# Kernel optimization log

Hardware: AMD Instinct MI355X
Metric: run time of the kernel (lower is better)

## Reference

```python
import jax, jax.numpy as jnp
import numpy as np

K = 3  # kernel size
PAD = 1  # padding (stride=1, dilation=1)


def _unfold(x, k=K, pad=PAD):
    """im2col: x [B,C,H,W] -> [B,C,k,k,H,W] (stride=1, dilation=1)."""
    B, C, H, W = x.shape
    xp = jnp.pad(x, ((0, 0), (0, 0), (pad, pad), (pad, pad)))
    # small fixed k*k loop, stacked into window dims
    rows = []
    for i in range(k):
        cols = [xp[:, :, i:i + H, j:j + W] for j in range(k)]
        rows.append(jnp.stack(cols, axis=2))  # [B,C,k,H,W]
    return jnp.stack(rows, axis=2)  # [B,C,k,k,H,W]


def setup_inputs() -> dict:
    key = jax.random.key(0)
    k1, k2, k3, k4 = jax.random.split(key, 4)
    B, C, O, H, W = 4, 64, 64, 128, 128
    inputs = jax.random.normal(k1, (B, C, H, W), dtype=jnp.float32)
    alpha = jax.random.uniform(k2, (B, 1, H, W), dtype=jnp.float32)
    fan_in = C * K * K
    weight = jax.random.normal(k3, (O, C, K, K), dtype=jnp.float32) / np.sqrt(fan_in)
    bias = jax.random.normal(k4, (O,), dtype=jnp.float32) / np.sqrt(fan_in)
    return {
        "inputs": inputs,
        "alpha": alpha,
        "weight": weight,
        "bias": bias,
        "a": jnp.float32(-4.0),
        "b": jnp.float32(4.0),
        "c": jnp.float32(1.0),
    }


def reference(inputs, alpha, weight, bias, a, b, c):
    # spatially-varying kernel from alpha: (a*x + b)*x + c on unfolded windows
    alpha_wins = _unfold(alpha)                      # [B,1,k,k,H,W]
    kernel = (a * alpha_wins + b) * alpha_wins + c   # [B,1,k,k,H,W]
    inputs_wins = _unfold(inputs)                    # [B,C,k,k,H,W]
    inputs_mul_kernel = inputs_wins * kernel         # broadcast over C
    out = jnp.einsum('ijklmn,ojkl->iomn', inputs_mul_kernel, weight)
    out = out + bias[None, :, None, None]
    return out
```

## Files before the change

kernel.cpp:

```cpp
#include <hip/hip_runtime.h>

typedef __bf16 bf16x8 __attribute__((ext_vector_type(8)));
typedef float f32x4 __attribute__((ext_vector_type(4)));

#define BB 4
#define CC 64
#define OO 64
#define HH 128
#define WW 128

__global__ __launch_bounds__(256) void prepack_kernel(
    const float* __restrict__ w, unsigned short* __restrict__ aw)
{
    int gid = blockIdx.x * 256 + threadIdx.x;
    if (gid >= 4608) return;
    int og  = gid / 1152;
    int rem = gid - og * 1152;
    int t = rem >> 6;
    int l = rem & 63;
    int q = l >> 4;
    int m = l & 15;
    int o  = og * 16 + m;
    int ij = t >> 1;
    int ch = t & 1;
    int i = ij / 3;
    int j = ij - i * 3;
    union { unsigned short u[8]; uint4 v; } pk;
#pragma unroll
    for (int jj = 0; jj < 8; ++jj) {
        int c = ch * 32 + q * 8 + jj;
        float wf = w[((o * CC + c) * 3 + i) * 3 + j];
        __bf16 h = (__bf16)wf;
        pk.u[jj] = __builtin_bit_cast(unsigned short, h);
    }
    ((uint4*)aw)[gid] = pk.v;
}

__global__ __launch_bounds__(256) void prescale_kernel(
    const float* __restrict__ in, const float* __restrict__ alpha,
    const float* __restrict__ pa, const float* __restrict__ pb, const float* __restrict__ pc,
    unsigned short* __restrict__ xs)
{
    __shared__ float trans[64][65];
    int bid = blockIdx.x;
    int xh  = bid & 1;
    int by  = bid >> 1;
    int y   = by & 127;
    int b   = by >> 7;
    int x0  = xh * 64;
    int tid = threadIdx.x;

    float A  = *pa, Bc = *pb, Cc = *pc;

    int x  = tid & 63;
    int c4 = tid >> 6;
    float av = alpha[(b * HH + y) * WW + x0 + x];
    float f  = (A * av + Bc) * av + Cc;
#pragma unroll
    for (int k = 0; k < 16; ++k) {
        int c = c4 * 16 + k;
        float v = in[((b * CC + c) * HH + y) * WW + x0 + x];
        trans[c][x] = v * f;
    }
    __syncthreads();

    int xw = tid >> 2;
    int cg = tid & 3;
    union { unsigned short u[16]; uint4 v4[2]; } pk;
#pragma unroll
    for (int k = 0; k < 16; ++k) {
        __bf16 h = (__bf16)trans[cg * 16 + k][xw];
        pk.u[k] = __builtin_bit_cast(unsigned short, h);
    }
    uint4* dst = (uint4*)(xs + (((size_t)(b * HH + y) * WW + x0 + xw) * CC + cg * 16));
    dst[0] = pk.v4[0];
    dst[1] = pk.v4[1];
}

__global__ __launch_bounds__(256, 2) void conv_kernel(
    const unsigned short* __restrict__ xs, const unsigned short* __restrict__ aw,
    const float* __restrict__ bias, float* __restrict__ out)
{
    __shared__ unsigned short tile[3 * 130 * 72];

    int n   = blockIdx.x;
    int xcd = n & 7;
    int idx = n >> 3;
    int b   = xcd >> 1;
    int y   = (xcd & 1) * 64 + idx;
    int tid = threadIdx.x;

    for (int s = tid; s < 3120; s += 256) {
        int g  = s & 7;
        int rx = s >> 3;
        int r  = rx / 130;
        int xt = rx - r * 130;
        int yy = y + r - 1;
        int xg = xt - 1;
        uint4 val = make_uint4(0u, 0u, 0u, 0u);
        if ((unsigned)yy < (unsigned)HH && (unsigned)xg < (unsigned)WW)
            val = *(const uint4*)(xs + (((size_t)(b * HH + yy) * WW + xg) * CC + g * 8));
        *(uint4*)(tile + (r * 130 + xt) * 72 + g * 8) = val;
    }
    __syncthreads();

    int wv = tid >> 6;
    int l  = tid & 63;
    int oh = wv & 1;
    int nh = wv >> 1;
    int q  = l >> 4;
    int m  = l & 15;

    f32x4 acc[2][4];
#pragma unroll
    for (int ag = 0; ag < 2; ++ag)
#pragma unroll
        for (int nf = 0; nf < 4; ++nf)
            acc[ag][nf] = (f32x4){0.f, 0.f, 0.f, 0.f};

    const uint4* awv = (const uint4*)aw + (size_t)(oh * 2) * 18 * 64 + l;

#pragma unroll 3
    for (int ij = 0; ij < 9; ++ij) {
        const int i = ij / 3;
        const int j = ij - i * 3;
#pragma unroll
        for (int ch = 0; ch < 2; ++ch) {
            const int t = ij * 2 + ch;
            bf16x8 afrag[2], bfrag[4];
#pragma unroll
            for (int ag = 0; ag < 2; ++ag)
                afrag[ag] = __builtin_bit_cast(bf16x8, awv[(ag * 18 + t) * 64]);
#pragma unroll
            for (int nf = 0; nf < 4; ++nf) {
                int xt = nh * 64 + nf * 16 + m + j;
                bfrag[nf] = __builtin_bit_cast(bf16x8,
                    *(const uint4*)(tile + (i * 130 + xt) * 72 + ch * 32 + q * 8));
            }
#pragma unroll
            for (int ag = 0; ag < 2; ++ag)
#pragma unroll
                for (int nf = 0; nf < 4; ++nf)
                    acc[ag][nf] = __builtin_amdgcn_mfma_f32_16x16x32_bf16(
                        afrag[ag], bfrag[nf], acc[ag][nf], 0, 0, 0);
        }
    }

#pragma unroll
    for (int ag = 0; ag < 2; ++ag) {
#pragma unroll
        for (int r = 0; r < 4; ++r) {
            int o = (oh * 2 + ag) * 16 + q * 4 + r;
            float bv = bias[o];
#pragma unroll
            for (int nf = 0; nf < 4; ++nf) {
                int x = nh * 64 + nf * 16 + m;
                out[((size_t)(b * OO + o) * HH + y) * WW + x] = acc[ag][nf][r] + bv;
            }
        }
    }
}

extern "C" void kernel_launch(void* const* d_in, const int* in_sizes, int n_in,
                              void* d_out, int out_size, void* d_ws, size_t ws_size,
                              hipStream_t stream) {
    const float* inputs = (const float*)d_in[0];
    const float* alpha  = (const float*)d_in[1];
    const float* weight = (const float*)d_in[2];
    const float* bias   = (const float*)d_in[3];
    const float* pa     = (const float*)d_in[4];
    const float* pb     = (const float*)d_in[5];
    const float* pc     = (const float*)d_in[6];
    float* out = (float*)d_out;

    unsigned short* aw = (unsigned short*)d_ws;
    unsigned short* xs = (unsigned short*)((char*)d_ws + 131072);

    prepack_kernel<<<18, 256, 0, stream>>>(weight, aw);
    prescale_kernel<<<BB * HH * 2, 256, 0, stream>>>(inputs, alpha, pa, pb, pc, xs);
    conv_kernel<<<BB * HH, 256, 0, stream>>>(xs, aw, bias, out);
}
```

Before: 96.45 us.

## Fuse alpha prescale and bf16 transpose into the conv kernel tile load

Removes the separate prescale kernel and its bf16 NHWC intermediate buffer. Each conv block now reads the three fp32 input rows directly, applies the alpha polynomial, transposes through a small shared buffer, and writes bf16 into the shared tile, with the halo columns zeroed explicitly. This saves a kernel launch and the intermediate write and read, but each input row is now loaded and converted by three blocks. The staging loop also adds 24 block-wide barriers with little overlap between loads and conversion.

```diff
diff --git a/kernel.cpp b/kernel.cpp
--- a/kernel.cpp
+++ b/kernel.cpp
@@ -36,52 +36,14 @@
     ((uint4*)aw)[gid] = pk.v;
 }
 
-__global__ __launch_bounds__(256) void prescale_kernel(
+__global__ __launch_bounds__(256, 2) void fused_conv_kernel(
     const float* __restrict__ in, const float* __restrict__ alpha,
+    const unsigned short* __restrict__ aw, const float* __restrict__ bias,
     const float* __restrict__ pa, const float* __restrict__ pb, const float* __restrict__ pc,
-    unsigned short* __restrict__ xs)
-{
-    __shared__ float trans[64][65];
-    int bid = blockIdx.x;
-    int xh  = bid & 1;
-    int by  = bid >> 1;
-    int y   = by & 127;
-    int b   = by >> 7;
-    int x0  = xh * 64;
-    int tid = threadIdx.x;
-
-    float A  = *pa, Bc = *pb, Cc = *pc;
-
-    int x  = tid & 63;
-    int c4 = tid >> 6;
-    float av = alpha[(b * HH + y) * WW + x0 + x];
-    float f  = (A * av + Bc) * av + Cc;
-#pragma unroll
-    for (int k = 0; k < 16; ++k) {
-        int c = c4 * 16 + k;
-        float v = in[((b * CC + c) * HH + y) * WW + x0 + x];
-        trans[c][x] = v * f;
-    }
-    __syncthreads();
-
-    int xw = tid >> 2;
-    int cg = tid & 3;
-    union { unsigned short u[16]; uint4 v4[2]; } pk;
-#pragma unroll
-    for (int k = 0; k < 16; ++k) {
-        __bf16 h = (__bf16)trans[cg * 16 + k][xw];
-        pk.u[k] = __builtin_bit_cast(unsigned short, h);
-    }
-    uint4* dst = (uint4*)(xs + (((size_t)(b * HH + y) * WW + x0 + xw) * CC + cg * 16));
-    dst[0] = pk.v4[0];
-    dst[1] = pk.v4[1];
-}
-
-__global__ __launch_bounds__(256, 2) void conv_kernel(
-    const unsigned short* __restrict__ xs, const unsigned short* __restrict__ aw,
-    const float* __restrict__ bias, float* __restrict__ out)
+    float* __restrict__ out)
 {
     __shared__ unsigned short tile[3 * 130 * 72];
+    __shared__ float trans[64][33];
 
     int n   = blockIdx.x;
     int xcd = n & 7;
@@ -90,19 +52,46 @@
     int y   = (xcd & 1) * 64 + idx;
     int tid = threadIdx.x;
 
-    for (int s = tid; s < 3120; s += 256) {
-        int g  = s & 7;
-        int rx = s >> 3;
-        int r  = rx / 130;
-        int xt = rx - r * 130;
+    float A  = *pa, Bc = *pb, Cc = *pc;
+
+    if (tid < 48) {
+        int g = tid & 7;
+        int e = (tid >> 3) & 1;
+        int r = tid >> 4;
+        int xt = e ? 129 : 0;
+        *(uint4*)(tile + (r * 130 + xt) * 72 + g * 8) = make_uint4(0u, 0u, 0u, 0u);
+    }
+
+    int xA = tid & 31, c8 = tid >> 5;
+    int xw = tid >> 3, cg = tid & 7;
+
+#pragma unroll
+    for (int r = 0; r < 3; ++r) {
         int yy = y + r - 1;
-        int xg = xt - 1;
-        uint4 val = make_uint4(0u, 0u, 0u, 0u);
-        if ((unsigned)yy < (unsigned)HH && (unsigned)xg < (unsigned)WW)
-            val = *(const uint4*)(xs + (((size_t)(b * HH + yy) * WW + xg) * CC + g * 8));
-        *(uint4*)(tile + (r * 130 + xt) * 72 + g * 8) = val;
+        bool inr = (0 <= yy) && (yy < HH);
+#pragma unroll
+        for (int xc = 0; xc < 4; ++xc) {
+            int x0 = xc * 32;
+            float av = inr ? alpha[(b * HH + yy) * WW + x0 + xA] : 0.f;
+            float f  = (A * av + Bc) * av + Cc;
+#pragma unroll
+            for (int k = 0; k < 8; ++k) {
+                int c = c8 * 8 + k;
+                float v = inr ? in[((b * CC + c) * HH + yy) * WW + x0 + xA] : 0.f;
+                trans[c][xA] = v * f;
+            }
+            __syncthreads();
+            union { unsigned short u[8]; uint4 v; } pk;
+#pragma unroll
+            for (int k = 0; k < 8; ++k) {
+                __bf16 h = (__bf16)trans[cg * 8 + k][xw];
+                pk.u[k] = __builtin_bit_cast(unsigned short, h);
+            }
+            int xt = x0 + xw + 1;
+            *(uint4*)(tile + (r * 130 + xt) * 72 + cg * 8) = pk.v;
+            __syncthreads();
+        }
     }
-    __syncthreads();
 
     int wv = tid >> 6;
     int l  = tid & 63;
@@ -174,9 +163,8 @@
     float* out = (float*)d_out;
 
     unsigned short* aw = (unsigned short*)d_ws;
-    unsigned short* xs = (unsigned short*)((char*)d_ws + 131072);
 
     prepack_kernel<<<18, 256, 0, stream>>>(weight, aw);
-    prescale_kernel<<<BB * HH * 2, 256, 0, stream>>>(inputs, alpha, pa, pb, pc, xs);
-    conv_kernel<<<BB * HH, 256, 0, stream>>>(xs, aw, bias, out);
+    fused_conv_kernel<<<BB * HH, 256, 0, stream>>>(inputs, alpha, aw, bias,
+                                                   pa, pb, pc, out);
 }
```

After: 106.0 us. 9.9% more time.
